# Performance work log

Hardware: AMD Instinct MI355X
Metric: run time of the kernel (lower is better)

The kernel has to match this reference:

```python
import jax, jax.numpy as jnp
import numpy as np

B, S, D, H, DFF, G = 2, 2048, 1024, 16, 4096, 64
HD = D // H  # seq_dimensions = d_model // num_heads
SCALE = 1.0 / np.sqrt(HD).astype(np.float32)


def _ln(x, g, b):
    m = x.mean(-1, keepdims=True)
    v = x.var(-1, keepdims=True)
    return (x - m) / jnp.sqrt(v + 1e-5) * g + b


def _mha(q_in, k_in, v_in, wq, bq, wk, bk, wv, bv, wo, bo, mask):
    Bq, Sq, _ = q_in.shape
    Sk = k_in.shape[1]
    def proj(t, w, b):
        return (t @ w + b).reshape(t.shape[0], t.shape[1], H, HD).transpose(0, 2, 1, 3)
    q = proj(q_in, wq, bq)  # [B,H,Sq,HD]
    k = proj(k_in, wk, bk)
    v = proj(v_in, wv, bv)
    scores = jnp.einsum('bhqd,bhkd->bhqk', q, k) * SCALE
    if mask is not None:
        scores = jnp.where(mask, scores, jnp.float32(-1e9))
    a = jax.nn.softmax(scores, axis=-1)
    o = jnp.einsum('bhqk,bhkd->bhqd', a, v).transpose(0, 2, 1, 3).reshape(Bq, Sq, D)
    return o @ wo + bo


def setup_inputs() -> dict:
    key = jax.random.key(0)
    ks = jax.random.split(key, 32)
    w = lambda i, shape: jax.random.normal(ks[i], shape, jnp.float32) * 0.02
    z = lambda shape: jnp.zeros(shape, jnp.float32)
    # BigBird-style mask: causal + global (first G tokens) + G random cols per row
    rng = np.random.default_rng(0)
    mask = np.tril(np.ones((S, S), dtype=bool))
    mask[:, :G] = True
    mask[:G, :] = True
    rand_cols = rng.integers(0, S, size=(S, G))
    mask[np.arange(S)[:, None], rand_cols] = True
    return dict(
        cur_input=jax.random.normal(ks[0], (B, S, D), jnp.float32),
        classVector=jax.random.normal(ks[1], (B, 1, 10), jnp.float32),
        attn_mask=jnp.asarray(mask),
        sa_wq=w(2, (D, D)), sa_bq=z(D), sa_wk=w(3, (D, D)), sa_bk=z(D),
        sa_wv=w(4, (D, D)), sa_bv=z(D), sa_wo=w(5, (D, D)), sa_bo=z(D),
        ln1_g=jnp.ones(D, jnp.float32), ln1_b=z(D),
        ce_w=w(6, (10, D)), ce_b=z(D),
        ca_wq=w(7, (D, D)), ca_bq=z(D), ca_wk=w(8, (D, D)), ca_bk=z(D),
        ca_wv=w(9, (D, D)), ca_bv=z(D), ca_wo=w(10, (D, D)), ca_bo=z(D),
        ln2_g=jnp.ones(D, jnp.float32), ln2_b=z(D),
        ff_w1=w(11, (D, DFF)), ff_b1=z(DFF), ff_w2=w(12, (DFF, D)), ff_b2=z(D),
        ln3_g=jnp.ones(D, jnp.float32), ln3_b=z(D),
    )


def reference(cur_input, classVector, attn_mask,
              sa_wq, sa_bq, sa_wk, sa_bk, sa_wv, sa_bv, sa_wo, sa_bo, ln1_g, ln1_b,
              ce_w, ce_b,
              ca_wq, ca_bq, ca_wk, ca_bk, ca_wv, ca_bv, ca_wo, ca_bo, ln2_g, ln2_b,
              ff_w1, ff_b1, ff_w2, ff_b2, ln3_g, ln3_b):
    # AddNorm(masked rand+global self-attn)
    sa = _mha(cur_input, cur_input, cur_input,
              sa_wq, sa_bq, sa_wk, sa_bk, sa_wv, sa_bv, sa_wo, sa_bo, attn_mask)
    h = _ln(cur_input + sa, ln1_g, ln1_b)
    # class vector embedding -> cross-attn K/V
    cv = classVector @ ce_w + ce_b  # [B,1,D]
    ca = _mha(h, cv, cv, ca_wq, ca_bq, ca_wk, ca_bk, ca_wv, ca_bv, ca_wo, ca_bo, None)
    h2 = _ln(h + ca, ln2_g, ln2_b)
    # AddNorm(FFN)
    ff = jax.nn.relu(h2 @ ff_w1 + ff_b1) @ ff_w2 + ff_b2
    return _ln(h2 + ff, ln3_g, ln3_b)
```

## Files before the change

kernel.cpp:

```cpp
#include <hip/hip_runtime.h>
#include <hip/hip_bf16.h>
#include <stdint.h>

#define S_LEN 2048
#define DMODEL 1024
#define NHEAD 16
#define BATCH 2

typedef __bf16 bf16x8 __attribute__((ext_vector_type(8)));
typedef __bf16 bf16x4 __attribute__((ext_vector_type(4)));
typedef float f32x4 __attribute__((ext_vector_type(4)));

__device__ __forceinline__ void gll16(const void* gsrc, void* ldst) {
  auto g = (const __attribute__((address_space(1))) unsigned int*)(uintptr_t)gsrc;
  auto l = (__attribute__((address_space(3))) unsigned int*)(uint32_t)(uintptr_t)ldst;
  __builtin_amdgcn_global_load_lds(g, l, 16, 0, 0);
}

__device__ __forceinline__ void wt_core(const float* __restrict__ W, __bf16* __restrict__ Wt,
                                        int Kd, int Nd, int bx, int by) {
  __shared__ __bf16 tile[64 * 72];
  const int n0 = bx * 64, k0 = by * 64;
  const int t = threadIdx.x;
#pragma unroll
  for (int i = 0; i < 16; ++i) {
    int idx = t + 256 * i;
    int r = idx >> 6, c = idx & 63;
    tile[r * 72 + c] = (__bf16)W[(size_t)(k0 + r) * Nd + n0 + c];
  }
  __syncthreads();
#pragma unroll
  for (int i = 0; i < 2; ++i) {
    int ch = t + 256 * i;
    int r = ch >> 3, c0 = (ch & 7) * 8;
    bf16x8 v;
#pragma unroll
    for (int j = 0; j < 8; ++j) v[j] = tile[(c0 + j) * 72 + r];
    *(bf16x8*)&Wt[(size_t)(n0 + r) * Kd + k0 + c0] = v;
  }
}

__global__ __launch_bounds__(256) void wt_kernel(const float* __restrict__ W,
                                                 __bf16* __restrict__ Wt, int Kd, int Nd) {
  wt_core(W, Wt, Kd, Nd, blockIdx.x, blockIdx.y);
}

__global__ __launch_bounds__(256) void wt4_kernel(const float* w0, const float* w1,
                                                  const float* w2, const float* w3, __bf16* o0,
                                                  __bf16* o1, __bf16* o2, __bf16* o3) {
  const int z = blockIdx.z;
  const float* W = (z == 0) ? w0 : (z == 1) ? w1 : (z == 2) ? w2 : w3;
  __bf16* Wt = (z == 0) ? o0 : (z == 1) ? o1 : (z == 2) ? o2 : o3;
  wt_core(W, Wt, 1024, 1024, blockIdx.x, blockIdx.y);
}

__global__ __launch_bounds__(256) void tobf_kernel(const float* __restrict__ x,
                                                   __bf16* __restrict__ y, int n4) {
  const int stride = gridDim.x * 256;
  for (int i = blockIdx.x * 256 + threadIdx.x; i < n4; i += stride) {
    float4 v = ((const float4*)x)[i];
    bf16x4 o = {(__bf16)v.x, (__bf16)v.y, (__bf16)v.z, (__bf16)v.w};
    *(bf16x4*)(y + (size_t)i * 4) = o;
  }
}

__global__ __launch_bounds__(256) void maskbits_kernel(const uint8_t* __restrict__ m8,
                                                       unsigned long long* __restrict__ mb) {
  const int idx = blockIdx.x * 256 + threadIdx.x;
  const int r = idx >> 5, c = idx & 31;
  const bool u8 = (m8[1] != 0);
  unsigned long long bits = 0;
  if (u8) {
    const unsigned long long* p = (const unsigned long long*)(m8 + (size_t)r * 2048 + c * 64);
#pragma unroll
    for (int i = 0; i < 8; ++i) {
      unsigned long long wq = p[i];
#pragma unroll
      for (int j = 0; j < 8; ++j)
        if ((wq >> (8 * j)) & 0xFFull) bits |= 1ull << (i * 8 + j);
    }
  } else {
    const int* p = (const int*)m8 + (size_t)r * 2048 + (size_t)c * 64;
#pragma unroll
    for (int i = 0; i < 64; ++i)
      if (p[i] != 0) bits |= 1ull << i;
  }
  mb[(size_t)r * 32 + c] = bits;
}

__device__ __forceinline__ void gemm_core(const __bf16* __restrict__ A,
                                          const __bf16* __restrict__ Bt,
                                          const float* __restrict__ bias,
                                          float* __restrict__ outF, __bf16* __restrict__ outB,
                                          bool relu, float scale, int N, int K) {
  __shared__ __bf16 As[2][128 * 64];
  __shared__ __bf16 Bs[2][128 * 64];
  const int t = threadIdx.x;
  const int l = t & 63, w = t >> 6;
  const int wr = w >> 1, wc = w & 1;
  const int gx = gridDim.x;
  const int lin = blockIdx.x + gx * blockIdx.y;
  const int cpx = (gx * gridDim.y) >> 3;
  const int s = (lin & 7) * cpx + (lin >> 3);
  const int bx = s % gx, by = s / gx;
  const int l15 = l & 15, l4 = l >> 4;
  f32x4 acc[4][4] = {};
  const size_t arow = (size_t)by * 128;
  const size_t brow = (size_t)bx * 128;

  auto stage = [&](int d, int k0) {
#pragma unroll
    for (int i = 0; i < 4; ++i) {
      int c = t + 256 * i;
      int r = c >> 3, sl = c & 7;
      int kk = (sl ^ (r & 7)) << 3;
      gll16(A + (arow + r) * K + k0 + kk, (char*)As[d] + (size_t)c * 16);
      gll16(Bt + (brow + r) * K + k0 + kk, (char*)Bs[d] + (size_t)c * 16);
    }
  };

  stage(0, 0);
  asm volatile("s_waitcnt vmcnt(0)" ::: "memory");
  __builtin_amdgcn_s_barrier();
  int cur = 0;
  for (int k0 = 0; k0 < K; k0 += 64) {
    if (k0 + 64 < K) stage(cur ^ 1, k0 + 64);
#pragma unroll
    for (int kk = 0; kk < 2; ++kk) {
      bf16x8 af[4], bfr[4];
#pragma unroll
      for (int m = 0; m < 4; ++m) {
        int row = wr * 64 + m * 16 + l15, vs = kk * 4 + l4;
        af[m] = *(const bf16x8*)((char*)As[cur] + row * 128 + ((vs ^ (row & 7)) << 4));
      }
#pragma unroll
      for (int n = 0; n < 4; ++n) {
        int row = wc * 64 + n * 16 + l15, vs = kk * 4 + l4;
        bfr[n] = *(const bf16x8*)((char*)Bs[cur] + row * 128 + ((vs ^ (row & 7)) << 4));
      }
#pragma unroll
      for (int m = 0; m < 4; ++m)
#pragma unroll
        for (int n = 0; n < 4; ++n)
          acc[m][n] = __builtin_amdgcn_mfma_f32_16x16x32_bf16(af[m], bfr[n], acc[m][n], 0, 0, 0);
    }
    asm volatile("s_waitcnt vmcnt(0)" ::: "memory");
    __builtin_amdgcn_s_barrier();
    cur ^= 1;
  }
  const int r0 = by * 128 + wr * 64, c0 = bx * 128 + wc * 64;
#pragma unroll
  for (int m = 0; m < 4; ++m) {
#pragma unroll
    for (int n = 0; n < 4; ++n) {
      int col = c0 + n * 16 + l15;
      float bv = bias ? bias[col] : 0.0f;
#pragma unroll
      for (int i = 0; i < 4; ++i) {
        int row = r0 + m * 16 + l4 * 4 + i;
        float v = (acc[m][n][i] + bv) * scale;
        if (relu) v = fmaxf(v, 0.0f);
        if (outF) outF[(size_t)row * N + col] = v;
        if (outB) outB[(size_t)row * N + col] = (__bf16)v;
      }
    }
  }
}

__global__ __launch_bounds__(256) void gemm_kernel(const __bf16* A, const __bf16* Bt,
                                                   const float* bias, float* outF, __bf16* outB,
                                                   int relu, float scale, int N, int K) {
  gemm_core(A, Bt, bias, outF, outB, relu != 0, scale, N, K);
}

__global__ __launch_bounds__(256) void gemm_qkv_kernel(const __bf16* A, const __bf16* WqT,
                                                       const __bf16* WkT, const __bf16* WvT,
                                                       const float* bq, const float* bk,
                                                       const float* bv, __bf16* Qo, __bf16* Ko,
                                                       __bf16* Vo) {
  const int z = blockIdx.z;
  const __bf16* Bt = (z == 0) ? WqT : (z == 1) ? WkT : WvT;
  const float* bias = (z == 0) ? bq : (z == 1) ? bk : bv;
  __bf16* out = (z == 0) ? Qo : (z == 1) ? Ko : Vo;
  const float scale = (z == 0) ? 0.125f : 1.0f;
  gemm_core(A, Bt, bias, nullptr, out, false, scale, DMODEL, DMODEL);
}

__global__ __launch_bounds__(256) void vt_kernel(const __bf16* __restrict__ V,
                                                 __bf16* __restrict__ Vt) {
  __shared__ __bf16 tile[64 * 72];
  const int sb = blockIdx.x, h = blockIdx.y, b = blockIdx.z;
  const int t = threadIdx.x;
#pragma unroll
  for (int i = 0; i < 2; ++i) {
    int ch = t + 256 * i;
    int r = ch >> 3, c0 = (ch & 7) * 8;
    *(bf16x8*)&tile[r * 72 + c0] =
        *(const bf16x8*)&V[(size_t)(b * S_LEN + sb * 64 + r) * DMODEL + h * 64 + c0];
  }
  __syncthreads();
#pragma unroll
  for (int i = 0; i < 2; ++i) {
    int ch = t + 256 * i;
    int r = ch >> 3, c0 = (ch & 7) * 8;
    bf16x8 v;
#pragma unroll
    for (int j = 0; j < 8; ++j) v[j] = tile[(c0 + j) * 72 + r];
    *(bf16x8*)&Vt[((size_t)((b * NHEAD + h) * 64) + r) * S_LEN + sb * 64 + c0] = v;
  }
}

__global__ __launch_bounds__(256, 4) void flash_kernel(const __bf16* __restrict__ Q,
                                                       const __bf16* __restrict__ K,
                                                       const __bf16* __restrict__ Vt,
                                                       const unsigned long long* __restrict__ mbits,
                                                       __bf16* __restrict__ O) {
  __shared__ char smem[40 * 1024];
  const int lin = blockIdx.x + 32 * (blockIdx.y + 16 * blockIdx.z);
  const int xr = lin & 7, xm = lin >> 3;
  const int g = xr + 8 * (xm & 3);
  const int qb = xm >> 2;
  const int h = g & 15, b = g >> 4;
  const int t = threadIdx.x, w = t >> 6, l = t & 63;
  const int l15 = l & 15, l4 = l >> 4;
  const int q_glob = qb * 64 + w * 16 + l15;

#pragma unroll
  for (int i = 0; i < 2; ++i) {
    int c = t + 256 * i;
    int r = c >> 3, p = c & 7;
    int vsl = p ^ (r & 7);
    gll16(Q + (size_t)(b * S_LEN + qb * 64 + r) * DMODEL + h * 64 + vsl * 8,
          smem + (size_t)c * 16);
    gll16(K + (size_t)(b * S_LEN + r) * DMODEL + h * 64 + vsl * 8, smem + 8192 + (size_t)c * 16);
    gll16(Vt + (size_t)((b * NHEAD + h) * 64 + r) * S_LEN + vsl * 8, smem + 24576 + (size_t)c * 16);
  }
  __syncthreads();

  bf16x8 aq[2];
#pragma unroll
  for (int ks = 0; ks < 2; ++ks) {
    int row = w * 16 + l15, vs = ks * 4 + l4;
    aq[ks] = *(const bf16x8*)(smem + row * 128 + ((vs ^ (row & 7)) << 4));
  }
  char* PsW = smem + w * 2048;

  f32x4 o[4] = {};
  float mrow = -INFINITY, lrow = 0.f;
  unsigned long long mb_cur = 0, mb_next = 0;
  int cur = 0;
  for (int kt = 0; kt < 32; ++kt) {
    char* Kc = smem + 8192 + cur * 8192;
    char* Vc = smem + 24576 + cur * 8192;
    if (kt < 31) {
      char* Kn = smem + 8192 + (cur ^ 1) * 8192;
      char* Vn = smem + 24576 + (cur ^ 1) * 8192;
#pragma unroll
      for (int i = 0; i < 2; ++i) {
        int c = t + 256 * i;
        int r = c >> 3, p = c & 7;
        int vsl = p ^ (r & 7);
        gll16(K + (size_t)(b * S_LEN + (kt + 1) * 64 + r) * DMODEL + h * 64 + vsl * 8,
              Kn + (size_t)c * 16);
        gll16(Vt + (size_t)((b * NHEAD + h) * 64 + r) * S_LEN + (kt + 1) * 64 + vsl * 8,
              Vn + (size_t)c * 16);
      }
      mb_next = mbits[(size_t)q_glob * 32 + kt + 1];
    }
    f32x4 s[4] = {};
#pragma unroll
    for (int ks = 0; ks < 2; ++ks)
#pragma unroll
      for (int n = 0; n < 4; ++n) {
        int row = n * 16 + l15, vs = ks * 4 + l4;
        bf16x8 kf = *(const bf16x8*)(Kc + row * 128 + ((vs ^ (row & 7)) << 4));
        s[n] = __builtin_amdgcn_mfma_f32_16x16x32_bf16(kf, aq[ks], s[n], 0, 0, 0);
      }
    const bool skip = (kt < qb) || (kt == 0) || (qb == 0);
    float tmax = s[0][0];
#pragma unroll
    for (int n = 0; n < 4; ++n)
#pragma unroll
      for (int i = 0; i < 4; ++i) tmax = fmaxf(tmax, s[n][i]);
    tmax = fmaxf(tmax, __shfl_xor(tmax, 16));
    tmax = fmaxf(tmax, __shfl_xor(tmax, 32));
    if (__ballot(tmax > mrow)) {
      const float nm = fmaxf(mrow, tmax);
      const float alpha = __expf(mrow - nm);
      mrow = nm;
      lrow *= alpha;
#pragma unroll
      for (int i = 0; i < 4; ++i) {
        float ai = __shfl(alpha, (l & 48) | (l4 * 4 + i));
#pragma unroll
        for (int n = 0; n < 4; ++n) o[n][i] *= ai;
      }
    }
    float pv[4][4];
#pragma unroll
    for (int n = 0; n < 4; ++n)
#pragma unroll
      for (int i = 0; i < 4; ++i) pv[n][i] = __expf(s[n][i] - mrow);
    if (!skip) {
#pragma unroll
      for (int n = 0; n < 4; ++n) {
        unsigned int mB = (unsigned int)(mb_cur >> (n * 16 + l4 * 4));
#pragma unroll
        for (int i = 0; i < 4; ++i)
          if (!((mB >> i) & 1)) pv[n][i] = 0.f;
      }
    }
    float tsum = 0.f;
#pragma unroll
    for (int n = 0; n < 4; ++n)
#pragma unroll
      for (int i = 0; i < 4; ++i) tsum += pv[n][i];
    tsum += __shfl_xor(tsum, 16);
    tsum += __shfl_xor(tsum, 32);
    lrow += tsum;
#pragma unroll
    for (int n = 0; n < 4; ++n) {
      bf16x4 pk = {(__bf16)pv[n][0], (__bf16)pv[n][1], (__bf16)pv[n][2], (__bf16)pv[n][3]};
      int slot = n * 4 + l4;
      *(bf16x4*)(PsW + l15 * 128 + ((slot ^ l15) & 15) * 8) = pk;
    }
#pragma unroll
    for (int ks = 0; ks < 2; ++ks) {
      int s0 = (ks * 8 + l4 * 2) ^ l15;
      int s1 = (ks * 8 + l4 * 2 + 1) ^ l15;
      bf16x4 pa0 = *(const bf16x4*)(PsW + l15 * 128 + s0 * 8);
      bf16x4 pa1 = *(const bf16x4*)(PsW + l15 * 128 + s1 * 8);
      bf16x8 ap = {pa0[0], pa0[1], pa0[2], pa0[3], pa1[0], pa1[1], pa1[2], pa1[3]};
#pragma unroll
      for (int n = 0; n < 4; ++n) {
        int vrow = n * 16 + l15, vvs = ks * 4 + l4;
        bf16x8 bv = *(const bf16x8*)(Vc + vrow * 128 + ((vvs ^ (vrow & 7)) << 4));
        o[n] = __builtin_amdgcn_mfma_f32_16x16x32_bf16(ap, bv, o[n], 0, 0, 0);
      }
    }
    asm volatile("s_waitcnt vmcnt(0)" ::: "memory");
    __builtin_amdgcn_s_barrier();
    mb_cur = mb_next;
    cur ^= 1;
  }
#pragma unroll
  for (int i = 0; i < 4; ++i) {
    float li = __shfl(lrow, (l & 48) | (l4 * 4 + i));
    float rli = 1.0f / li;
#pragma unroll
    for (int n = 0; n < 4; ++n)
      O[(size_t)(b * S_LEN + qb * 64 + w * 16 + l4 * 4 + i) * DMODEL + h * 64 + n * 16 + l15] =
          (__bf16)(o[n][i] * rli);
  }
}

__global__ __launch_bounds__(256) void ln_kernel(const float* __restrict__ x,
                                                 const float* __restrict__ res,
                                                 const float* __restrict__ resvec,
                                                 const float* __restrict__ g,
                                                 const float* __restrict__ beta,
                                                 float* __restrict__ outF,
                                                 __bf16* __restrict__ outB) {
  const int row = blockIdx.x;
  const int b = row >> 11;
  const int t = threadIdx.x;
  float4 v = ((const float4*)(x + (size_t)row * DMODEL))[t];
  if (res) {
    float4 r = ((const float4*)(res + (size_t)row * DMODEL))[t];
    v.x += r.x; v.y += r.y; v.z += r.z; v.w += r.w;
  }
  if (resvec) {
    float4 r = ((const float4*)(resvec + (size_t)b * DMODEL))[t];
    v.x += r.x; v.y += r.y; v.z += r.z; v.w += r.w;
  }
  float s1 = v.x + v.y + v.z + v.w;
  float s2 = v.x * v.x + v.y * v.y + v.z * v.z + v.w * v.w;
#pragma unroll
  for (int off = 32; off; off >>= 1) {
    s1 += __shfl_xor(s1, off);
    s2 += __shfl_xor(s2, off);
  }
  __shared__ float red[8];
  const int w = t >> 6, l = t & 63;
  if (l == 0) { red[w] = s1; red[4 + w] = s2; }
  __syncthreads();
  s1 = red[0] + red[1] + red[2] + red[3];
  s2 = red[4] + red[5] + red[6] + red[7];
  const float mean = s1 * (1.0f / DMODEL);
  const float var = s2 * (1.0f / DMODEL) - mean * mean;
  const float rstd = rsqrtf(var + 1e-5f);
  float4 gg = ((const float4*)g)[t];
  float4 bb = ((const float4*)beta)[t];
  float4 o;
  o.x = (v.x - mean) * rstd * gg.x + bb.x;
  o.y = (v.y - mean) * rstd * gg.y + bb.y;
  o.z = (v.z - mean) * rstd * gg.z + bb.z;
  o.w = (v.w - mean) * rstd * gg.w + bb.w;
  if (outF) ((float4*)(outF + (size_t)row * DMODEL))[t] = o;
  if (outB) {
    bf16x4 p = {(__bf16)o.x, (__bf16)o.y, (__bf16)o.z, (__bf16)o.w};
    *(bf16x4*)(outB + (size_t)row * DMODEL + t * 4) = p;
  }
}

__global__ __launch_bounds__(256) void cv_kernel(const float* __restrict__ cls,
                                                 const float* __restrict__ cw,
                                                 const float* __restrict__ cb,
                                                 float* __restrict__ cv) {
  const int i = blockIdx.x * 256 + threadIdx.x;
  const int b = i >> 10, d = i & 1023;
  float s = cb[d];
#pragma unroll
  for (int j = 0; j < 10; ++j) s += cls[b * 10 + j] * cw[j * DMODEL + d];
  cv[i] = s;
}

__global__ __launch_bounds__(256) void matvec_part_kernel(const float* __restrict__ x,
                                                          const float* __restrict__ W,
                                                          float* __restrict__ part) {
  const int c = blockIdx.x, b = blockIdx.y;
  const int t = threadIdx.x;
  float4 acc = {0.f, 0.f, 0.f, 0.f};
  const int k0 = c * 16;
#pragma unroll
  for (int k = 0; k < 16; ++k) {
    float xv = x[b * DMODEL + k0 + k];
    float4 wv = ((const float4*)(W + (size_t)(k0 + k) * DMODEL))[t];
    acc.x += xv * wv.x; acc.y += xv * wv.y; acc.z += xv * wv.z; acc.w += xv * wv.w;
  }
  ((float4*)(part + ((size_t)(b * 64 + c)) * DMODEL))[t] = acc;
}

__global__ __launch_bounds__(256) void matvec_red_kernel(const float* __restrict__ part,
                                                         const float* __restrict__ bias,
                                                         float* __restrict__ out) {
  const int b = blockIdx.y;
  const int t = threadIdx.x;
  float4 acc = ((const float4*)bias)[t];
#pragma unroll 8
  for (int c = 0; c < 64; ++c) {
    float4 p = ((const float4*)(part + ((size_t)(b * 64 + c)) * DMODEL))[t];
    acc.x += p.x; acc.y += p.y; acc.z += p.z; acc.w += p.w;
  }
  ((float4*)(out + (size_t)b * DMODEL))[t] = acc;
}

extern "C" void kernel_launch(void* const* d_in, const int* in_sizes, int n_in, void* d_out,
                              int out_size, void* d_ws, size_t ws_size, hipStream_t stream) {
  (void)in_sizes; (void)n_in; (void)out_size; (void)ws_size;
  const float* cur = (const float*)d_in[0];
  const float* cls = (const float*)d_in[1];
  const uint8_t* msk = (const uint8_t*)d_in[2];
  const float* sa_wq = (const float*)d_in[3];
  const float* sa_bq = (const float*)d_in[4];
  const float* sa_wk = (const float*)d_in[5];
  const float* sa_bk = (const float*)d_in[6];
  const float* sa_wv = (const float*)d_in[7];
  const float* sa_bv = (const float*)d_in[8];
  const float* sa_wo = (const float*)d_in[9];
  const float* sa_bo = (const float*)d_in[10];
  const float* ln1_g = (const float*)d_in[11];
  const float* ln1_b = (const float*)d_in[12];
  const float* ce_w = (const float*)d_in[13];
  const float* ce_b = (const float*)d_in[14];
  const float* ca_wv = (const float*)d_in[19];
  const float* ca_bv = (const float*)d_in[20];
  const float* ca_wo = (const float*)d_in[21];
  const float* ca_bo = (const float*)d_in[22];
  const float* ln2_g = (const float*)d_in[23];
  const float* ln2_b = (const float*)d_in[24];
  const float* ff_w1 = (const float*)d_in[25];
  const float* ff_b1 = (const float*)d_in[26];
  const float* ff_w2 = (const float*)d_in[27];
  const float* ff_b2 = (const float*)d_in[28];
  const float* ln3_g = (const float*)d_in[29];
  const float* ln3_b = (const float*)d_in[30];

  char* ws = (char*)d_ws;
  const size_t MB = 1ull << 20;
  __bf16* WQT = (__bf16*)(ws + 0 * MB);
  __bf16* WKT = (__bf16*)(ws + 2 * MB);
  __bf16* WVT = (__bf16*)(ws + 4 * MB);
  __bf16* WOT = (__bf16*)(ws + 6 * MB);
  __bf16* W1T = (__bf16*)(ws + 8 * MB);
  __bf16* W2T = (__bf16*)(ws + 16 * MB);
  __bf16* XBF = (__bf16*)(ws + 24 * MB);
  __bf16* QBF = (__bf16*)(ws + 32 * MB);
  __bf16* KBF = (__bf16*)(ws + 40 * MB);
  __bf16* VBF = (__bf16*)(ws + 48 * MB);
  __bf16* VTT = (__bf16*)(ws + 56 * MB);
  __bf16* F1 = (__bf16*)(ws + 32 * MB);
  float* ATT = (float*)(ws + 64 * MB);
  float* HF = (float*)(ws + 80 * MB);
  float* H2F = (float*)(ws + 96 * MB);
  __bf16* H2B = (__bf16*)(ws + 112 * MB);
  float* CVV = (float*)(ws + 120 * MB);
  float* VV = (float*)(ws + 120 * MB + 65536);
  float* CAV = (float*)(ws + 120 * MB + 131072);
  unsigned long long* MBITS = (unsigned long long*)(ws + 121 * MB);
  float* MVP = (float*)(ws + 122 * MB);

  dim3 blk(256);
  maskbits_kernel<<<dim3(256), blk, 0, stream>>>(msk, MBITS);
  wt4_kernel<<<dim3(16, 16, 4), blk, 0, stream>>>(sa_wq, sa_wk, sa_wv, sa_wo, WQT, WKT, WVT, WOT);
  wt_kernel<<<dim3(64, 16), blk, 0, stream>>>(ff_w1, W1T, 1024, 4096);
  wt_kernel<<<dim3(16, 64), blk, 0, stream>>>(ff_w2, W2T, 4096, 1024);
  tobf_kernel<<<dim3(2048), blk, 0, stream>>>(cur, XBF, 1048576);
  gemm_qkv_kernel<<<dim3(8, 32, 3), blk, 0, stream>>>(XBF, WQT, WKT, WVT, sa_bq, sa_bk, sa_bv,
                                                      QBF, KBF, VBF);
  vt_kernel<<<dim3(32, 16, 2), blk, 0, stream>>>(VBF, VTT);
  flash_kernel<<<dim3(32, 16, 2), blk, 0, stream>>>(QBF, KBF, VTT, MBITS, XBF);
  gemm_kernel<<<dim3(8, 32), blk, 0, stream>>>(XBF, WOT, sa_bo, ATT, nullptr, 0, 1.0f, 1024, 1024);
  ln_kernel<<<dim3(4096), blk, 0, stream>>>(cur, ATT, nullptr, ln1_g, ln1_b, HF, nullptr);
  cv_kernel<<<dim3(8), blk, 0, stream>>>(cls, ce_w, ce_b, CVV);
  matvec_part_kernel<<<dim3(64, 2), blk, 0, stream>>>(CVV, ca_wv, MVP);
  matvec_red_kernel<<<dim3(1, 2), blk, 0, stream>>>(MVP, ca_bv, VV);
  matvec_part_kernel<<<dim3(64, 2), blk, 0, stream>>>(VV, ca_wo, MVP);
  matvec_red_kernel<<<dim3(1, 2), blk, 0, stream>>>(MVP, ca_bo, CAV);
  ln_kernel<<<dim3(4096), blk, 0, stream>>>(HF, nullptr, CAV, ln2_g, ln2_b, H2F, H2B);
  gemm_kernel<<<dim3(32, 32), blk, 0, stream>>>(H2B, W1T, ff_b1, nullptr, F1, 1, 1.0f, 4096, 1024);
  gemm_kernel<<<dim3(8, 32), blk, 0, stream>>>(F1, W2T, ff_b2, ATT, nullptr, 0, 1.0f, 1024, 4096);
  ln_kernel<<<dim3(4096), blk, 0, stream>>>(H2F, ATT, nullptr, ln3_g, ln3_b, (float*)d_out,
                                            nullptr);
}
```

Baseline: 321.4 us.

## Process two 64-row query blocks per flash attention workgroup to reuse K/V tiles

Each flash-attention workgroup now handles 128 query rows (two 64-row halves) instead of 64, so every K/V tile loaded into shared memory serves twice as many queries. This halves global K/V traffic and the number of blocks (512 instead of 1024). Shared memory grows to 48KB, register use doubles for accumulators, and the occupancy hint drops from 4 to 3 waves, so there is less parallelism to hide latency.

```diff
diff --git a/kernel.cpp b/kernel.cpp
--- a/kernel.cpp
+++ b/kernel.cpp
@@ -210,51 +210,60 @@
   }
 }
 
-__global__ __launch_bounds__(256, 4) void flash_kernel(const __bf16* __restrict__ Q,
+__global__ __launch_bounds__(256, 3) void flash_kernel(const __bf16* __restrict__ Q,
                                                        const __bf16* __restrict__ K,
                                                        const __bf16* __restrict__ Vt,
                                                        const unsigned long long* __restrict__ mbits,
                                                        __bf16* __restrict__ O) {
-  __shared__ char smem[40 * 1024];
-  const int lin = blockIdx.x + 32 * (blockIdx.y + 16 * blockIdx.z);
+  __shared__ char smem[48 * 1024];
+  const int lin = blockIdx.x + 16 * (blockIdx.y + 16 * blockIdx.z);
   const int xr = lin & 7, xm = lin >> 3;
   const int g = xr + 8 * (xm & 3);
   const int qb = xm >> 2;
   const int h = g & 15, b = g >> 4;
   const int t = threadIdx.x, w = t >> 6, l = t & 63;
   const int l15 = l & 15, l4 = l >> 4;
-  const int q_glob = qb * 64 + w * 16 + l15;
-
+  const int qg0 = qb * 128 + w * 16 + l15;
+  const int qg1 = qg0 + 64;
+
+#pragma unroll
+  for (int i = 0; i < 4; ++i) {
+    int c = t + 256 * i;
+    int r = c >> 3, p = c & 7;
+    int vsl = p ^ (r & 7);
+    gll16(Q + (size_t)(b * S_LEN + qb * 128 + r) * DMODEL + h * 64 + vsl * 8,
+          smem + (size_t)c * 16);
+  }
 #pragma unroll
   for (int i = 0; i < 2; ++i) {
     int c = t + 256 * i;
     int r = c >> 3, p = c & 7;
     int vsl = p ^ (r & 7);
-    gll16(Q + (size_t)(b * S_LEN + qb * 64 + r) * DMODEL + h * 64 + vsl * 8,
-          smem + (size_t)c * 16);
-    gll16(K + (size_t)(b * S_LEN + r) * DMODEL + h * 64 + vsl * 8, smem + 8192 + (size_t)c * 16);
-    gll16(Vt + (size_t)((b * NHEAD + h) * 64 + r) * S_LEN + vsl * 8, smem + 24576 + (size_t)c * 16);
+    gll16(K + (size_t)(b * S_LEN + r) * DMODEL + h * 64 + vsl * 8, smem + 16384 + (size_t)c * 16);
+    gll16(Vt + (size_t)((b * NHEAD + h) * 64 + r) * S_LEN + vsl * 8, smem + 32768 + (size_t)c * 16);
   }
   __syncthreads();
 
-  bf16x8 aq[2];
-#pragma unroll
-  for (int ks = 0; ks < 2; ++ks) {
-    int row = w * 16 + l15, vs = ks * 4 + l4;
-    aq[ks] = *(const bf16x8*)(smem + row * 128 + ((vs ^ (row & 7)) << 4));
-  }
-  char* PsW = smem + w * 2048;
-
-  f32x4 o[4] = {};
-  float mrow = -INFINITY, lrow = 0.f;
-  unsigned long long mb_cur = 0, mb_next = 0;
+  bf16x8 aq[2][2];
+#pragma unroll
+  for (int qh = 0; qh < 2; ++qh)
+#pragma unroll
+    for (int ks = 0; ks < 2; ++ks) {
+      int row = qh * 64 + w * 16 + l15, vs = ks * 4 + l4;
+      aq[qh][ks] = *(const bf16x8*)(smem + row * 128 + ((vs ^ (row & 7)) << 4));
+    }
+  char* PsW[2] = {smem + w * 2048, smem + 8192 + w * 2048};
+
+  f32x4 o[2][4] = {};
+  float mrow[2] = {-INFINITY, -INFINITY}, lrow[2] = {0.f, 0.f};
+  unsigned long long mb_cur[2] = {0, 0}, mb_next[2] = {0, 0};
   int cur = 0;
   for (int kt = 0; kt < 32; ++kt) {
-    char* Kc = smem + 8192 + cur * 8192;
-    char* Vc = smem + 24576 + cur * 8192;
+    char* Kc = smem + 16384 + cur * 8192;
+    char* Vc = smem + 32768 + cur * 8192;
     if (kt < 31) {
-      char* Kn = smem + 8192 + (cur ^ 1) * 8192;
-      char* Vn = smem + 24576 + (cur ^ 1) * 8192;
+      char* Kn = smem + 16384 + (cur ^ 1) * 8192;
+      char* Vn = smem + 32768 + (cur ^ 1) * 8192;
 #pragma unroll
       for (int i = 0; i < 2; ++i) {
         int c = t + 256 * i;
@@ -265,93 +274,101 @@
         gll16(Vt + (size_t)((b * NHEAD + h) * 64 + r) * S_LEN + (kt + 1) * 64 + vsl * 8,
               Vn + (size_t)c * 16);
       }
-      mb_next = mbits[(size_t)q_glob * 32 + kt + 1];
-    }
-    f32x4 s[4] = {};
-#pragma unroll
-    for (int ks = 0; ks < 2; ++ks)
+      mb_next[0] = mbits[(size_t)qg0 * 32 + kt + 1];
+      mb_next[1] = mbits[(size_t)qg1 * 32 + kt + 1];
+    }
+#pragma unroll
+    for (int qh = 0; qh < 2; ++qh) {
+      f32x4 s[4] = {};
+#pragma unroll
+      for (int ks = 0; ks < 2; ++ks)
+#pragma unroll
+        for (int n = 0; n < 4; ++n) {
+          int row = n * 16 + l15, vs = ks * 4 + l4;
+          bf16x8 kf = *(const bf16x8*)(Kc + row * 128 + ((vs ^ (row & 7)) << 4));
+          s[n] = __builtin_amdgcn_mfma_f32_16x16x32_bf16(kf, aq[qh][ks], s[n], 0, 0, 0);
+        }
+      const int qrb = 2 * qb + qh;
+      const bool skip = (kt < qrb) || (kt == 0) || (qrb == 0);
+      float tmax = s[0][0];
+#pragma unroll
+      for (int n = 0; n < 4; ++n)
+#pragma unroll
+        for (int i = 0; i < 4; ++i) tmax = fmaxf(tmax, s[n][i]);
+      tmax = fmaxf(tmax, __shfl_xor(tmax, 16));
+      tmax = fmaxf(tmax, __shfl_xor(tmax, 32));
+      if (__ballot(tmax > mrow[qh])) {
+        const float nm = fmaxf(mrow[qh], tmax);
+        const float alpha = __expf(mrow[qh] - nm);
+        mrow[qh] = nm;
+        lrow[qh] *= alpha;
+#pragma unroll
+        for (int i = 0; i < 4; ++i) {
+          float ai = __shfl(alpha, (l & 48) | (l4 * 4 + i));
+#pragma unroll
+          for (int n = 0; n < 4; ++n) o[qh][n][i] *= ai;
+        }
+      }
+      float pv[4][4];
+#pragma unroll
+      for (int n = 0; n < 4; ++n)
+#pragma unroll
+        for (int i = 0; i < 4; ++i) pv[n][i] = __expf(s[n][i] - mrow[qh]);
+      if (!skip) {
+#pragma unroll
+        for (int n = 0; n < 4; ++n) {
+          unsigned int mB = (unsigned int)(mb_cur[qh] >> (n * 16 + l4 * 4));
+#pragma unroll
+          for (int i = 0; i < 4; ++i)
+            if (!((mB >> i) & 1)) pv[n][i] = 0.f;
+        }
+      }
+      float tsum = 0.f;
+#pragma unroll
+      for (int n = 0; n < 4; ++n)
+#pragma unroll
+        for (int i = 0; i < 4; ++i) tsum += pv[n][i];
+      tsum += __shfl_xor(tsum, 16);
+      tsum += __shfl_xor(tsum, 32);
+      lrow[qh] += tsum;
 #pragma unroll
       for (int n = 0; n < 4; ++n) {
-        int row = n * 16 + l15, vs = ks * 4 + l4;
-        bf16x8 kf = *(const bf16x8*)(Kc + row * 128 + ((vs ^ (row & 7)) << 4));
-        s[n] = __builtin_amdgcn_mfma_f32_16x16x32_bf16(kf, aq[ks], s[n], 0, 0, 0);
-      }
-    const bool skip = (kt < qb) || (kt == 0) || (qb == 0);
-    float tmax = s[0][0];
-#pragma unroll
-    for (int n = 0; n < 4; ++n)
-#pragma unroll
-      for (int i = 0; i < 4; ++i) tmax = fmaxf(tmax, s[n][i]);
-    tmax = fmaxf(tmax, __shfl_xor(tmax, 16));
-    tmax = fmaxf(tmax, __shfl_xor(tmax, 32));
-    if (__ballot(tmax > mrow)) {
-      const float nm = fmaxf(mrow, tmax);
-      const float alpha = __expf(mrow - nm);
-      mrow = nm;
-      lrow *= alpha;
-#pragma unroll
-      for (int i = 0; i < 4; ++i) {
-        float ai = __shfl(alpha, (l & 48) | (l4 * 4 + i));
-#pragma unroll
-        for (int n = 0; n < 4; ++n) o[n][i] *= ai;
-      }
-    }
-    float pv[4][4];
-#pragma unroll
-    for (int n = 0; n < 4; ++n)
-#pragma unroll
-      for (int i = 0; i < 4; ++i) pv[n][i] = __expf(s[n][i] - mrow);
-    if (!skip) {
-#pragma unroll
-      for (int n = 0; n < 4; ++n) {
-        unsigned int mB = (unsigned int)(mb_cur >> (n * 16 + l4 * 4));
-#pragma unroll
-        for (int i = 0; i < 4; ++i)
-          if (!((mB >> i) & 1)) pv[n][i] = 0.f;
-      }
-    }
-    float tsum = 0.f;
-#pragma unroll
-    for (int n = 0; n < 4; ++n)
-#pragma unroll
-      for (int i = 0; i < 4; ++i) tsum += pv[n][i];
-    tsum += __shfl_xor(tsum, 16);
-    tsum += __shfl_xor(tsum, 32);
-    lrow += tsum;
-#pragma unroll
-    for (int n = 0; n < 4; ++n) {
-      bf16x4 pk = {(__bf16)pv[n][0], (__bf16)pv[n][1], (__bf16)pv[n][2], (__bf16)pv[n][3]};
-      int slot = n * 4 + l4;
-      *(bf16x4*)(PsW + l15 * 128 + ((slot ^ l15) & 15) * 8) = pk;
-    }
-#pragma unroll
-    for (int ks = 0; ks < 2; ++ks) {
-      int s0 = (ks * 8 + l4 * 2) ^ l15;
-      int s1 = (ks * 8 + l4 * 2 + 1) ^ l15;
-      bf16x4 pa0 = *(const bf16x4*)(PsW + l15 * 128 + s0 * 8);
-      bf16x4 pa1 = *(const bf16x4*)(PsW + l15 * 128 + s1 * 8);
-      bf16x8 ap = {pa0[0], pa0[1], pa0[2], pa0[3], pa1[0], pa1[1], pa1[2], pa1[3]};
-#pragma unroll
-      for (int n = 0; n < 4; ++n) {
-        int vrow = n * 16 + l15, vvs = ks * 4 + l4;
-        bf16x8 bv = *(const bf16x8*)(Vc + vrow * 128 + ((vvs ^ (vrow & 7)) << 4));
-        o[n] = __builtin_amdgcn_mfma_f32_16x16x32_bf16(ap, bv, o[n], 0, 0, 0);
+        bf16x4 pk = {(__bf16)pv[n][0], (__bf16)pv[n][1], (__bf16)pv[n][2], (__bf16)pv[n][3]};
+        int slot = n * 4 + l4;
+        *(bf16x4*)(PsW[qh] + l15 * 128 + ((slot ^ l15) & 15) * 8) = pk;
+      }
+#pragma unroll
+      for (int ks = 0; ks < 2; ++ks) {
+        int s0 = (ks * 8 + l4 * 2) ^ l15;
+        int s1 = (ks * 8 + l4 * 2 + 1) ^ l15;
+        bf16x4 pa0 = *(const bf16x4*)(PsW[qh] + l15 * 128 + (s0 & 15) * 8);
+        bf16x4 pa1 = *(const bf16x4*)(PsW[qh] + l15 * 128 + (s1 & 15) * 8);
+        bf16x8 ap = {pa0[0], pa0[1], pa0[2], pa0[3], pa1[0], pa1[1], pa1[2], pa1[3]};
+#pragma unroll
+        for (int n = 0; n < 4; ++n) {
+          int vrow = n * 16 + l15, vvs = ks * 4 + l4;
+          bf16x8 bv = *(const bf16x8*)(Vc + vrow * 128 + ((vvs ^ (vrow & 7)) << 4));
+          o[qh][n] = __builtin_amdgcn_mfma_f32_16x16x32_bf16(ap, bv, o[qh][n], 0, 0, 0);
+        }
       }
     }
     asm volatile("s_waitcnt vmcnt(0)" ::: "memory");
     __builtin_amdgcn_s_barrier();
-    mb_cur = mb_next;
+    mb_cur[0] = mb_next[0];
+    mb_cur[1] = mb_next[1];
     cur ^= 1;
   }
 #pragma unroll
-  for (int i = 0; i < 4; ++i) {
-    float li = __shfl(lrow, (l & 48) | (l4 * 4 + i));
-    float rli = 1.0f / li;
-#pragma unroll
-    for (int n = 0; n < 4; ++n)
-      O[(size_t)(b * S_LEN + qb * 64 + w * 16 + l4 * 4 + i) * DMODEL + h * 64 + n * 16 + l15] =
-          (__bf16)(o[n][i] * rli);
-  }
+  for (int qh = 0; qh < 2; ++qh)
+#pragma unroll
+    for (int i = 0; i < 4; ++i) {
+      float li = __shfl(lrow[qh], (l & 48) | (l4 * 4 + i));
+      float rli = 1.0f / li;
+#pragma unroll
+      for (int n = 0; n < 4; ++n)
+        O[(size_t)(b * S_LEN + qb * 128 + qh * 64 + w * 16 + l4 * 4 + i) * DMODEL + h * 64 +
+          n * 16 + l15] = (__bf16)(o[qh][n][i] * rli);
+    }
 }
 
 __global__ __launch_bounds__(256) void ln_kernel(const float* __restrict__ x,
@@ -509,7 +526,7 @@
   gemm_qkv_kernel<<<dim3(8, 32, 3), blk, 0, stream>>>(XBF, WQT, WKT, WVT, sa_bq, sa_bk, sa_bv,
                                                       QBF, KBF, VBF);
   vt_kernel<<<dim3(32, 16, 2), blk, 0, stream>>>(VBF, VTT);
-  flash_kernel<<<dim3(32, 16, 2), blk, 0, stream>>>(QBF, KBF, VTT, MBITS, XBF);
+  flash_kernel<<<dim3(16, 16, 2), blk, 0, stream>>>(QBF, KBF, VTT, MBITS, XBF);
   gemm_kernel<<<dim3(8, 32), blk, 0, stream>>>(XBF, WOT, sa_bo, ATT, nullptr, 0, 1.0f, 1024, 1024);
   ln_kernel<<<dim3(4096), blk, 0, stream>>>(cur, ATT, nullptr, ln1_g, ln1_b, HF, nullptr);
   cv_kernel<<<dim3(8), blk, 0, stream>>>(cls, ce_w, ce_b, CVV);
```

Measured after the change: 324.3 us. No clear change (+0.9%).
